# Optimization experiments

Hardware: AMD Instinct MI355X
Metric: run time of the kernel (lower is better)

The kernel has to match this reference:

```python
import jax, jax.numpy as jnp
import numpy as np

NODE_DEG = 9   # SelfAttnAggregation.node_degree: 8 grid neighbors + self loop
PN_EPS = 1e-5  # PyG PairNorm default eps


def _pairnorm(x):
    # PairNorm mode='PN', scale=1: center over nodes, divide by sqrt(mean row sq-norm)
    x = x - x.mean(axis=0, keepdims=True)
    return x / jnp.sqrt(PN_EPS + (x * x).sum(-1).mean())


def _mha(z, qkv_w, qkv_b, out_w, out_b):
    # torch.nn.MultiheadAttention, 1 head, batch_first. z: [N, S, E]
    E = z.shape[-1]
    qkv = jnp.einsum('nse,fe->nsf', z, qkv_w) + qkv_b            # [N, S, 3E]
    q, k, v = jnp.split(qkv, 3, axis=-1)
    scores = jnp.einsum('nse,nte->nst', q, k) / jnp.sqrt(jnp.asarray(E, z.dtype))
    o = jnp.einsum('nst,nte->nse', jax.nn.softmax(scores, axis=-1), v)
    return jnp.einsum('nse,fe->nsf', o, out_w) + out_b


def _gcn_conv(x, W, b, nbr_idx, qkv_w, qkv_b, out_w, out_b):
    # GCNConv(normalize=False, add_self_loops baked into nbr_idx) + SelfAttnAggregation
    h = x @ W                                   # [N, C]
    C = h.shape[-1]
    dense = h[nbr_idx]                          # [N, 9, C]  to_dense_batch gather
    N, S, _ = dense.shape
    pos = jnp.broadcast_to(jnp.eye(S, dtype=h.dtype), (N, S, S))
    z = jnp.concatenate([dense, pos], axis=-1)  # [N, 9, C+9]; pad amount is 0 for deg==9
    z = z + _mha(z, qkv_w[0], qkv_b[0], out_w[0], out_b[0]) \
          + _mha(z, qkv_w[1], qkv_b[1], out_w[1], out_b[1])
    return jnp.max(z[:, :, :C], axis=1) + b     # max-pool over neighbor slots, then bias


def setup_inputs() -> dict:
    key = jax.random.key(0)
    N, HID, W = 32768, 80, 80
    E = W + NODE_DEG  # 89
    ks = jax.random.split(key, 6)
    x = jax.random.normal(ks[0], (N, HID + 2), jnp.float32)
    nbr = jax.random.randint(ks[1], (N, NODE_DEG), 0, N, dtype=jnp.int32)
    nbr = nbr.at[:, -1].set(jnp.arange(N, dtype=jnp.int32))  # add_self_loops=True
    s = 0.05
    return {
        'x': x,
        'W1': jax.random.normal(ks[2], (HID + 2, W), jnp.float32) * s,
        'b1': jnp.zeros((W,), jnp.float32),
        'W2': jax.random.normal(ks[3], (W, W), jnp.float32) * s,
        'b2': jnp.zeros((W,), jnp.float32),
        'attn_qkv_w': jax.random.normal(ks[4], (2, 2, 3 * E, E), jnp.float32) * s,
        'attn_qkv_b': jnp.zeros((2, 2, 3 * E), jnp.float32),
        'attn_out_w': jax.random.normal(ks[5], (2, 2, E, E), jnp.float32) * s,
        'attn_out_b': jnp.zeros((2, 2, E), jnp.float32),
        'nbr_idx': nbr,
    }


def reference(x, W1, b1, W2, b2, attn_qkv_w, attn_qkv_b, attn_out_w, attn_out_b, nbr_idx):
    # UpdateRule.step()
    u = _gcn_conv(x, W1, b1, nbr_idx, attn_qkv_w[0], attn_qkv_b[0], attn_out_w[0], attn_out_b[0])
    u = jax.nn.relu(_pairnorm(u))
    u = _gcn_conv(u, W2, b2, nbr_idx, attn_qkv_w[1], attn_qkv_b[1], attn_out_w[1], attn_out_b[1])
    u = jax.nn.relu(_pairnorm(u))
    out = x[:, :-2] + u                          # residual (drops the 2 flag channels)
    last = out[:, -1]
    last = jnp.where((last > 1.0) | (last < -1.0), 0.0, last)
    out = out.at[:, -1].set(last)
    return out * 0.5
```

## Files before the change

### kernel.cpp

```cpp
#include <hip/hip_runtime.h>

#define NN 32768
#define HWID 448

#define OFF_G     0
#define OFF_M     25600
#define OFF_FF    51200
#define OFF_FG    54080
#define OFF_CC    56960
#define OFF_C2    57284
#define OFF_CW    60164
#define OFF_STATS 133636
#define OFF_MS    133956
#define OFF_H     134148
#define OFF_U     14814212

__global__ __launch_bounds__(256) void k_prep_small(const float* __restrict__ qkvw,
                                                    const float* __restrict__ qkvb,
                                                    const float* __restrict__ outw,
                                                    float* __restrict__ ws) {
    int combo = blockIdx.y;
    int e = blockIdx.x * 256 + threadIdx.x;
    const float* Wq = qkvw + combo * 267 * 89;
    const float* Wk = Wq + 89 * 89;
    const float* Wv = Wq + 178 * 89;
    const float* bq = qkvb + combo * 267;
    const float* bk = bq + 89;
    const float* bv = bq + 178;
    const float* Wo = outw + combo * 89 * 89;
    if (e < 6400) {
        int a = e / 80, b = e % 80;
        float s = 0.f;
        for (int j = 0; j < 89; ++j) s += Wq[j*89+a] * Wk[j*89+b];
        ws[OFF_G + combo*6400 + e] = s;
    } else if (e < 12800) {
        int e2 = e - 6400; int f = e2 / 80, c = e2 % 80;
        float s = 0.f;
        for (int j = 0; j < 89; ++j) s += Wo[f*89+j] * Wv[j*89+c];
        ws[OFF_M + combo*6400 + e2] = s;
    } else if (e < 13520) {
        int e3 = e - 12800; int a = e3 / 9, t = e3 % 9;
        float s = 0.f;
        for (int j = 0; j < 89; ++j) s += Wq[j*89+a] * (Wk[j*89+80+t] + bk[j]);
        ws[OFF_FF + combo*720 + e3] = s;
    } else if (e < 14240) {
        int e4 = e - 13520; int a = e4 / 9, si = e4 % 9;
        float s = 0.f;
        for (int j = 0; j < 89; ++j) s += Wk[j*89+a] * (Wq[j*89+80+si] + bq[j]);
        ws[OFF_FG + combo*720 + e4] = s;
    } else if (e < 14321) {
        int e5 = e - 14240; int si = e5 / 9, t = e5 % 9;
        float s = 0.f;
        for (int j = 0; j < 89; ++j) s += (Wq[j*89+80+si] + bq[j]) * (Wk[j*89+80+t] + bk[j]);
        ws[OFF_CC + combo*81 + e5] = s;
    } else if (e < 15041) {
        int e6 = e - 14321; int t = e6 / 80, f = e6 % 80;
        float s = 0.f;
        for (int j = 0; j < 89; ++j) s += Wo[f*89+j] * (Wv[j*89+80+t] + bv[j]);
        ws[OFF_C2 + combo*720 + e6] = s;
    }
}

__global__ __launch_bounds__(256) void k_prep_cw(const float* __restrict__ W1,
                                                 const float* __restrict__ W2,
                                                 float* __restrict__ ws) {
    int l = blockIdx.y;
    int e = blockIdx.x * 256 + threadIdx.x;
    if (e >= 82 * 448) return;
    int k = e / 448, j = e % 448;
    int K = (l == 0) ? 82 : 80;
    float val = 0.f;
    if (k < K) {
        const float* Wr = ((l == 0) ? W1 : W2) + k * 80;
        if (j < 80) {
            val = Wr[j];
        } else if (j < 240) {
            int m = (j - 80) / 80, col = (j - 80) % 80;
            const float* G = ws + OFF_G + (l*2+m)*6400;
            float s = 0.f;
            for (int c = 0; c < 80; ++c) s += Wr[c] * G[c*80 + col];
            val = s;
        } else if (j < 276) {
            int q = j - 240; int m = q / 18; int qq = q % 18;
            int combo = l*2 + m;
            if (qq < 9) {
                const float* Ff = ws + OFF_FF + combo*720;
                float s = 0.f;
                for (int c = 0; c < 80; ++c) s += Wr[c] * Ff[c*9 + qq];
                val = s;
            } else {
                const float* Fg = ws + OFF_FG + combo*720;
                float s = 0.f;
                for (int c = 0; c < 80; ++c) s += Wr[c] * Fg[c*9 + qq - 9];
                val = s;
            }
        } else if (j >= 280 && j < 440) {
            int m = (j - 280) / 80, f = (j - 280) % 80;
            const float* M = ws + OFF_M + (l*2+m)*6400 + f*80;
            float s = 0.f;
            for (int c = 0; c < 80; ++c) s += Wr[c] * M[c];
            val = s;
        }
    }
    ws[OFF_CW + (size_t)l*82*448 + e] = val;
}

template<int K, bool TRANS>
__global__ __launch_bounds__(256) void k_gemm(const float* __restrict__ A,
                                              const float* __restrict__ CW,
                                              float* __restrict__ H,
                                              const float* __restrict__ ms) {
    __shared__ __align__(16) float AsT[K][72];
    __shared__ __align__(16) float Bs[K][68];
    int tid = threadIdx.x;
    int n0 = blockIdx.x * 64;
    int j0 = blockIdx.y * 64;
    float scale0 = 0.f;
    if constexpr (TRANS) scale0 = ms[80];
    for (int idx = tid; idx < 64 * K; idx += 256) {
        int r = idx / K, k = idx - r * K;
        float v = A[(size_t)(n0 + r) * K + k];
        if constexpr (TRANS) v = fmaxf(0.f, (v - ms[k]) * scale0);
        AsT[k][r] = v;
    }
    for (int idx = tid; idx < K * 16; idx += 256) {
        int k = idx >> 4, c4 = idx & 15;
        *(float4*)(&Bs[k][c4 * 4]) = *(const float4*)(&CW[k * 448 + j0 + c4 * 4]);
    }
    __syncthreads();
    int r0 = (tid >> 4) * 4, c0 = (tid & 15) * 4;
    float acc[4][4] = {};
    #pragma unroll 2
    for (int k = 0; k < K; ++k) {
        float4 a4 = *(const float4*)(&AsT[k][r0]);
        float4 b4 = *(const float4*)(&Bs[k][c0]);
        acc[0][0] += a4.x*b4.x; acc[0][1] += a4.x*b4.y; acc[0][2] += a4.x*b4.z; acc[0][3] += a4.x*b4.w;
        acc[1][0] += a4.y*b4.x; acc[1][1] += a4.y*b4.y; acc[1][2] += a4.y*b4.z; acc[1][3] += a4.y*b4.w;
        acc[2][0] += a4.z*b4.x; acc[2][1] += a4.z*b4.y; acc[2][2] += a4.z*b4.z; acc[2][3] += a4.z*b4.w;
        acc[3][0] += a4.w*b4.x; acc[3][1] += a4.w*b4.y; acc[3][2] += a4.w*b4.z; acc[3][3] += a4.w*b4.w;
    }
    for (int i = 0; i < 4; ++i) {
        float4 v = make_float4(acc[i][0], acc[i][1], acc[i][2], acc[i][3]);
        *(float4*)(&H[(size_t)(n0 + r0 + i) * HWID + j0 + c0]) = v;
    }
}

__global__ __launch_bounds__(128) void k_attn(const float* __restrict__ ws,
                                              const float* __restrict__ Hbuf,
                                              const int* __restrict__ nbr,
                                              const float* __restrict__ outb,
                                              const float* __restrict__ bvec,
                                              float* __restrict__ u,
                                              int l) {
    __shared__ __align__(16) float sS[2][9][242];
    __shared__ float sP[2][2][9][9];
    __shared__ float sCC[2][81];
    int tid = threadIdx.x;
    int wave = tid >> 6, lane = tid & 63;
    int n = blockIdx.x * 2 + wave;
    int nv = nbr[n * 9 + (lane < 9 ? lane : 8)];
    int rr[9];
    #pragma unroll
    for (int s = 0; s < 9; ++s) rr[s] = __shfl(nv, s);

    int s1 = lane / 9, t1 = lane - s1 * 9;
    const float* rowS1 = Hbuf + (size_t)rr[s1] * HWID;
    const float* rowT1 = Hbuf + (size_t)rr[t1] * HWID;
    float f1a = rowS1[240 + t1], g1a = rowT1[249 + s1];
    float f2a = rowS1[258 + t1], g2a = rowT1[267 + s1];
    int pp2 = (lane < 17) ? (lane + 64) : 80;
    int s2 = pp2 / 9, t2 = pp2 - s2 * 9;
    const float* rowS2 = Hbuf + (size_t)rr[s2] * HWID;
    const float* rowT2 = Hbuf + (size_t)rr[t2] * HWID;
    float f1b = rowS2[240 + t2], g1b = rowT2[249 + s2];
    float f2b = rowS2[258 + t2], g2b = rowT2[267 + s2];

    for (int i = tid; i < 162; i += 128) sCC[0][i] = ws[OFF_CC + (l*2)*81 + i];

    float4 st0, st1, st2, st3, st4, st5, st6, st7, st8;
    {
        #define LD_ST(J, DST)                                                   \
        {   int i = lane + 64 * (J);                                            \
            int row = i / 60, c4 = i - row * 60;                                \
            int r = __shfl(nv, row);                                            \
            if (i < 540) DST = *(const float4*)(Hbuf + (size_t)r * HWID + c4 * 4); \
            else DST = make_float4(0.f,0.f,0.f,0.f); }
        LD_ST(0, st0) LD_ST(1, st1) LD_ST(2, st2) LD_ST(3, st3) LD_ST(4, st4)
        LD_ST(5, st5) LD_ST(6, st6) LD_ST(7, st7) LD_ST(8, st8)
        #undef LD_ST
    }
    {
        #define ST_ST(J, SRC)                                                   \
        {   int i = lane + 64 * (J);                                            \
            if (i < 540) {                                                      \
                int row = i / 60, c4 = i - row * 60;                            \
                *(float4*)(&sS[wave][row][c4 * 4]) = SRC; } }
        ST_ST(0, st0) ST_ST(1, st1) ST_ST(2, st2) ST_ST(3, st3) ST_ST(4, st4)
        ST_ST(5, st5) ST_ST(6, st6) ST_ST(7, st7) ST_ST(8, st8)
        #undef ST_ST
    }
    __syncthreads();

    const float rsE = 1.0f / 9.433981132056603f;
    {
        float a0 = 0.f, a1 = 0.f, b0 = 0.f, b1 = 0.f;
        #pragma unroll
        for (int i = 0; i < 20; ++i) {
            float4 hh = *(const float4*)(&sS[wave][t1][4*i]);
            float4 g1 = *(const float4*)(&sS[wave][s1][80 + 4*i]);
            float4 g2 = *(const float4*)(&sS[wave][s1][160 + 4*i]);
            a0 += g1.x*hh.x + g1.y*hh.y; a1 += g1.z*hh.z + g1.w*hh.w;
            b0 += g2.x*hh.x + g2.y*hh.y; b1 += g2.z*hh.z + g2.w*hh.w;
        }
        sP[wave][0][s1][t1] = (a0 + a1 + f1a + g1a + sCC[0][lane]) * rsE;
        sP[wave][1][s1][t1] = (b0 + b1 + f2a + g2a + sCC[1][lane]) * rsE;
    }
    if (lane < 17) {
        float a0 = 0.f, a1 = 0.f, b0 = 0.f, b1 = 0.f;
        #pragma unroll
        for (int i = 0; i < 20; ++i) {
            float4 hh = *(const float4*)(&sS[wave][t2][4*i]);
            float4 g1 = *(const float4*)(&sS[wave][s2][80 + 4*i]);
            float4 g2 = *(const float4*)(&sS[wave][s2][160 + 4*i]);
            a0 += g1.x*hh.x + g1.y*hh.y; a1 += g1.z*hh.z + g1.w*hh.w;
            b0 += g2.x*hh.x + g2.y*hh.y; b1 += g2.z*hh.z + g2.w*hh.w;
        }
        sP[wave][0][s2][t2] = (a0 + a1 + f1b + g1b + sCC[0][pp2]) * rsE;
        sP[wave][1][s2][t2] = (b0 + b1 + f2b + g2b + sCC[1][pp2]) * rsE;
    }
    __syncthreads();
    if (lane < 18) {
        int m = lane / 9, s = lane - m*9;
        float row[9]; float mx = -1e30f;
        #pragma unroll
        for (int t = 0; t < 9; ++t) { row[t] = sP[wave][m][s][t]; mx = fmaxf(mx, row[t]); }
        float sm = 0.f;
        #pragma unroll
        for (int t = 0; t < 9; ++t) { row[t] = __expf(row[t] - mx); sm += row[t]; }
        float inv = 1.f / sm;
        #pragma unroll
        for (int t = 0; t < 9; ++t) sP[wave][m][s][t] = row[t] * inv;
    }
    __syncthreads();
    for (int f = lane; f < 80; f += 64) {
        float acc[9] = {};
        #pragma unroll
        for (int m = 0; m < 2; ++m) {
            const float* c2 = ws + OFF_C2 + (l*2+m)*720;
            #pragma unroll
            for (int t = 0; t < 9; ++t) {
                float vv = Hbuf[(size_t)rr[t]*HWID + 280 + m*80 + f] + c2[t*80 + f];
                #pragma unroll
                for (int s = 0; s < 9; ++s) acc[s] += sP[wave][m][s][t] * vv;
            }
        }
        float mx = -1e30f;
        #pragma unroll
        for (int s = 0; s < 9; ++s) mx = fmaxf(mx, acc[s] + sS[wave][s][f]);
        float bias = outb[(l*2)*89 + f] + outb[(l*2+1)*89 + f] + bvec[f];
        u[(size_t)n*80 + f] = mx + bias;
    }
}

__global__ __launch_bounds__(256) void k_colreduce(const float* __restrict__ u, float* __restrict__ stats) {
    __shared__ float ps[3][80], ps2[3][80];
    int tid = threadIdx.x;
    int c = tid % 80, rg = tid / 80;
    if (rg < 3) {
        float s = 0.f, s2 = 0.f;
        int rbase = blockIdx.x * 48 + rg * 16;
        for (int i = 0; i < 16; ++i) {
            int rw = rbase + i;
            if (rw < NN) {
                float v = u[(size_t)rw*80 + c];
                s += v; s2 += v*v;
            }
        }
        ps[rg][c] = s; ps2[rg][c] = s2;
    }
    __syncthreads();
    if (tid < 80) {
        atomicAdd(&stats[tid],      ps[0][tid] + ps[1][tid] + ps[2][tid]);
        atomicAdd(&stats[80 + tid], ps2[0][tid] + ps2[1][tid] + ps2[2][tid]);
    }
}

__global__ __launch_bounds__(128) void k_normscale(const float* __restrict__ stats, float* __restrict__ ms) {
    __shared__ float red[80];
    int t = threadIdx.x;
    if (t < 80) {
        float mean = stats[t] * (1.0f / (float)NN);
        ms[t] = mean;
        red[t] = stats[80 + t] - (float)NN * mean * mean;
    }
    __syncthreads();
    if (t == 0) {
        float ss = 0.f;
        for (int i = 0; i < 80; ++i) ss += red[i];
        ms[80] = 1.0f / sqrtf(1e-5f + ss * (1.0f / (float)NN));
    }
}

__global__ __launch_bounds__(256) void k_final(const float* __restrict__ x,
                                               const float* __restrict__ u2,
                                               const float* __restrict__ ms,
                                               float* __restrict__ out) {
    int g = blockIdx.x * 256 + threadIdx.x;
    int n = g / 80, f = g % 80;
    float scale0 = ms[80];
    float v = fmaxf(0.f, (u2[g] - ms[f]) * scale0);
    float o = x[(size_t)n*82 + f] + v;
    if (f == 79 && (o > 1.0f || o < -1.0f)) o = 0.f;
    out[g] = o * 0.5f;
}

extern "C" void kernel_launch(void* const* d_in, const int* in_sizes, int n_in,
                              void* d_out, int out_size, void* d_ws, size_t ws_size,
                              hipStream_t stream) {
    const float* x    = (const float*)d_in[0];
    const float* W1   = (const float*)d_in[1];
    const float* b1   = (const float*)d_in[2];
    const float* W2   = (const float*)d_in[3];
    const float* b2   = (const float*)d_in[4];
    const float* qkvw = (const float*)d_in[5];
    const float* qkvb = (const float*)d_in[6];
    const float* outw = (const float*)d_in[7];
    const float* outb = (const float*)d_in[8];
    const int*   nbr  = (const int*)d_in[9];
    float* ws = (float*)d_ws;
    float* out = (float*)d_out;

    float* H = ws + OFF_H;
    float* u = ws + OFF_U;

    hipMemsetAsync(ws + OFF_STATS, 0, 320 * sizeof(float), stream);
    k_prep_small<<<dim3(59, 4), 256, 0, stream>>>(qkvw, qkvb, outw, ws);
    k_prep_cw<<<dim3(144, 2), 256, 0, stream>>>(W1, W2, ws);

    k_gemm<82, false><<<dim3(512, 7), 256, 0, stream>>>(x, ws + OFF_CW, H, nullptr);
    k_attn<<<16384, 128, 0, stream>>>(ws, H, nbr, outb, b1, u, 0);
    k_colreduce<<<683, 256, 0, stream>>>(u, ws + OFF_STATS);
    k_normscale<<<1, 128, 0, stream>>>(ws + OFF_STATS, ws + OFF_MS);

    k_gemm<80, true><<<dim3(512, 7), 256, 0, stream>>>(u, ws + OFF_CW + 82*448, H, ws + OFF_MS);
    k_attn<<<16384, 128, 0, stream>>>(ws, H, nbr, outb, b2, u, 1);
    k_colreduce<<<683, 256, 0, stream>>>(u, ws + OFF_STATS + 160);
    k_normscale<<<1, 128, 0, stream>>>(ws + OFF_STATS + 160, ws + OFF_MS + 96);

    k_final<<<10240, 256, 0, stream>>>(x, u, ws + OFF_MS + 96, out);
}
```

Before: 523.1 us.

## Split attention heads across waves with one node per block in k_attn

The attention kernel now handles one node per 128-thread block instead of two, and each wave computes one of the two attention heads. Gathering the 9 neighbor rows is shared by both waves, each wave computes scores for a single head, and the final stage splits the 80 output features 40 per wave. V-values and bias are loaded into registers before the first barrier so their latency overlaps the shared-memory fill. The launch grid doubles, block-level barriers now couple two waves of the same node, and 24 lanes per wave sit idle in the output stage.

Result: no change. 524.9 us (+0.3%).

```diff
diff --git a/kernel.cpp b/kernel.cpp
--- a/kernel.cpp
+++ b/kernel.cpp
@@ -152,112 +152,113 @@
                                               const float* __restrict__ bvec,
                                               float* __restrict__ u,
                                               int l) {
-    __shared__ __align__(16) float sS[2][9][242];
-    __shared__ float sP[2][2][9][9];
-    __shared__ float sCC[2][81];
+    __shared__ __align__(16) float sS[9][242];
+    __shared__ float sP[2][9][9];
     int tid = threadIdx.x;
-    int wave = tid >> 6, lane = tid & 63;
-    int n = blockIdx.x * 2 + wave;
+    int m = tid >> 6, lane = tid & 63;
+    int n = blockIdx.x;
     int nv = nbr[n * 9 + (lane < 9 ? lane : 8)];
     int rr[9];
     #pragma unroll
     for (int s = 0; s < 9; ++s) rr[s] = __shfl(nv, s);
 
+    int pp2 = (lane < 17) ? (lane + 64) : 80;
     int s1 = lane / 9, t1 = lane - s1 * 9;
+    int s2 = pp2 / 9, t2 = pp2 - s2 * 9;
+
     const float* rowS1 = Hbuf + (size_t)rr[s1] * HWID;
     const float* rowT1 = Hbuf + (size_t)rr[t1] * HWID;
-    float f1a = rowS1[240 + t1], g1a = rowT1[249 + s1];
-    float f2a = rowS1[258 + t1], g2a = rowT1[267 + s1];
-    int pp2 = (lane < 17) ? (lane + 64) : 80;
-    int s2 = pp2 / 9, t2 = pp2 - s2 * 9;
+    float fa = rowS1[240 + 18*m + t1], ga = rowT1[249 + 18*m + s1];
     const float* rowS2 = Hbuf + (size_t)rr[s2] * HWID;
     const float* rowT2 = Hbuf + (size_t)rr[t2] * HWID;
-    float f1b = rowS2[240 + t2], g1b = rowT2[249 + s2];
-    float f2b = rowS2[258 + t2], g2b = rowT2[267 + s2];
-
-    for (int i = tid; i < 162; i += 128) sCC[0][i] = ws[OFF_CC + (l*2)*81 + i];
-
-    float4 st0, st1, st2, st3, st4, st5, st6, st7, st8;
+    float fb = rowS2[240 + 18*m + t2], gb = rowT2[249 + 18*m + s2];
+
+    float cca = ws[OFF_CC + (l*2 + m)*81 + lane];
+    float ccb = ws[OFF_CC + (l*2 + m)*81 + pp2];
+
+    float4 st0, st1, st2, st3, st4;
     {
         #define LD_ST(J, DST)                                                   \
-        {   int i = lane + 64 * (J);                                            \
+        {   int i = tid + 128 * (J);                                            \
             int row = i / 60, c4 = i - row * 60;                                \
-            int r = __shfl(nv, row);                                            \
-            if (i < 540) DST = *(const float4*)(Hbuf + (size_t)r * HWID + c4 * 4); \
-            else DST = make_float4(0.f,0.f,0.f,0.f); }
+            if (i < 540) {                                                      \
+                int r = __shfl(nv, row);                                        \
+                DST = *(const float4*)(Hbuf + (size_t)r * HWID + c4 * 4);       \
+            } else DST = make_float4(0.f,0.f,0.f,0.f); }
         LD_ST(0, st0) LD_ST(1, st1) LD_ST(2, st2) LD_ST(3, st3) LD_ST(4, st4)
-        LD_ST(5, st5) LD_ST(6, st6) LD_ST(7, st7) LD_ST(8, st8)
         #undef LD_ST
     }
     {
         #define ST_ST(J, SRC)                                                   \
-        {   int i = lane + 64 * (J);                                            \
+        {   int i = tid + 128 * (J);                                            \
             if (i < 540) {                                                      \
                 int row = i / 60, c4 = i - row * 60;                            \
-                *(float4*)(&sS[wave][row][c4 * 4]) = SRC; } }
+                *(float4*)(&sS[row][c4 * 4]) = SRC; } }
         ST_ST(0, st0) ST_ST(1, st1) ST_ST(2, st2) ST_ST(3, st3) ST_ST(4, st4)
-        ST_ST(5, st5) ST_ST(6, st6) ST_ST(7, st7) ST_ST(8, st8)
         #undef ST_ST
     }
+
+    int f = 40*m + ((lane < 40) ? lane : 39);
+    const float* c20 = ws + OFF_C2 + (l*2)*720;
+    const float* c21 = c20 + 720;
+    float v0[9], v1[9];
+    #pragma unroll
+    for (int t = 0; t < 9; ++t) {
+        const float* rowp = Hbuf + (size_t)rr[t] * HWID + 280;
+        v0[t] = rowp[f]      + c20[t*80 + f];
+        v1[t] = rowp[80 + f] + c21[t*80 + f];
+    }
+    float bias = outb[(l*2)*89 + f] + outb[(l*2+1)*89 + f] + bvec[f];
+
     __syncthreads();
 
     const float rsE = 1.0f / 9.433981132056603f;
+    int goff = 80 + 80*m;
     {
-        float a0 = 0.f, a1 = 0.f, b0 = 0.f, b1 = 0.f;
+        float a0 = 0.f, a1 = 0.f;
         #pragma unroll
         for (int i = 0; i < 20; ++i) {
-            float4 hh = *(const float4*)(&sS[wave][t1][4*i]);
-            float4 g1 = *(const float4*)(&sS[wave][s1][80 + 4*i]);
-            float4 g2 = *(const float4*)(&sS[wave][s1][160 + 4*i]);
-            a0 += g1.x*hh.x + g1.y*hh.y; a1 += g1.z*hh.z + g1.w*hh.w;
-            b0 += g2.x*hh.x + g2.y*hh.y; b1 += g2.z*hh.z + g2.w*hh.w;
-        }
-        sP[wave][0][s1][t1] = (a0 + a1 + f1a + g1a + sCC[0][lane]) * rsE;
-        sP[wave][1][s1][t1] = (b0 + b1 + f2a + g2a + sCC[1][lane]) * rsE;
+            float4 hh = *(const float4*)(&sS[t1][4*i]);
+            float4 gg = *(const float4*)(&sS[s1][goff + 4*i]);
+            a0 += gg.x*hh.x + gg.y*hh.y; a1 += gg.z*hh.z + gg.w*hh.w;
+        }
+        sP[m][s1][t1] = (a0 + a1 + fa + ga + cca) * rsE;
     }
     if (lane < 17) {
-        float a0 = 0.f, a1 = 0.f, b0 = 0.f, b1 = 0.f;
+        float a0 = 0.f, a1 = 0.f;
         #pragma unroll
         for (int i = 0; i < 20; ++i) {
-            float4 hh = *(const float4*)(&sS[wave][t2][4*i]);
-            float4 g1 = *(const float4*)(&sS[wave][s2][80 + 4*i]);
-            float4 g2 = *(const float4*)(&sS[wave][s2][160 + 4*i]);
-            a0 += g1.x*hh.x + g1.y*hh.y; a1 += g1.z*hh.z + g1.w*hh.w;
-            b0 += g2.x*hh.x + g2.y*hh.y; b1 += g2.z*hh.z + g2.w*hh.w;
-        }
-        sP[wave][0][s2][t2] = (a0 + a1 + f1b + g1b + sCC[0][pp2]) * rsE;
-        sP[wave][1][s2][t2] = (b0 + b1 + f2b + g2b + sCC[1][pp2]) * rsE;
-    }
-    __syncthreads();
-    if (lane < 18) {
-        int m = lane / 9, s = lane - m*9;
+            float4 hh = *(const float4*)(&sS[t2][4*i]);
+            float4 gg = *(const float4*)(&sS[s2][goff + 4*i]);
+            a0 += gg.x*hh.x + gg.y*hh.y; a1 += gg.z*hh.z + gg.w*hh.w;
+        }
+        sP[m][s2][t2] = (a0 + a1 + fb + gb + ccb) * rsE;
+    }
+    __syncthreads();
+    if (lane < 9) {
+        int s = lane;
         float row[9]; float mx = -1e30f;
         #pragma unroll
-        for (int t = 0; t < 9; ++t) { row[t] = sP[wave][m][s][t]; mx = fmaxf(mx, row[t]); }
+        for (int t = 0; t < 9; ++t) { row[t] = sP[m][s][t]; mx = fmaxf(mx, row[t]); }
         float sm = 0.f;
         #pragma unroll
         for (int t = 0; t < 9; ++t) { row[t] = __expf(row[t] - mx); sm += row[t]; }
         float inv = 1.f / sm;
         #pragma unroll
-        for (int t = 0; t < 9; ++t) sP[wave][m][s][t] = row[t] * inv;
-    }
-    __syncthreads();
-    for (int f = lane; f < 80; f += 64) {
+        for (int t = 0; t < 9; ++t) sP[m][s][t] = row[t] * inv;
+    }
+    __syncthreads();
+    if (lane < 40) {
         float acc[9] = {};
         #pragma unroll
-        for (int m = 0; m < 2; ++m) {
-            const float* c2 = ws + OFF_C2 + (l*2+m)*720;
+        for (int t = 0; t < 9; ++t) {
+            float a = v0[t], b = v1[t];
             #pragma unroll
-            for (int t = 0; t < 9; ++t) {
-                float vv = Hbuf[(size_t)rr[t]*HWID + 280 + m*80 + f] + c2[t*80 + f];
-                #pragma unroll
-                for (int s = 0; s < 9; ++s) acc[s] += sP[wave][m][s][t] * vv;
-            }
+            for (int s = 0; s < 9; ++s) acc[s] += sP[0][s][t] * a + sP[1][s][t] * b;
         }
         float mx = -1e30f;
         #pragma unroll
-        for (int s = 0; s < 9; ++s) mx = fmaxf(mx, acc[s] + sS[wave][s][f]);
-        float bias = outb[(l*2)*89 + f] + outb[(l*2+1)*89 + f] + bvec[f];
+        for (int s = 0; s < 9; ++s) mx = fmaxf(mx, acc[s] + sS[s][f]);
         u[(size_t)n*80 + f] = mx + bias;
     }
 }
@@ -338,12 +339,12 @@
     k_prep_cw<<<dim3(144, 2), 256, 0, stream>>>(W1, W2, ws);
 
     k_gemm<82, false><<<dim3(512, 7), 256, 0, stream>>>(x, ws + OFF_CW, H, nullptr);
-    k_attn<<<16384, 128, 0, stream>>>(ws, H, nbr, outb, b1, u, 0);
+    k_attn<<<32768, 128, 0, stream>>>(ws, H, nbr, outb, b1, u, 0);
     k_colreduce<<<683, 256, 0, stream>>>(u, ws + OFF_STATS);
     k_normscale<<<1, 128, 0, stream>>>(ws + OFF_STATS, ws + OFF_MS);
 
     k_gemm<80, true><<<dim3(512, 7), 256, 0, stream>>>(u, ws + OFF_CW + 82*448, H, ws + OFF_MS);
-    k_attn<<<16384, 128, 0, stream>>>(ws, H, nbr, outb, b2, u, 1);
+    k_attn<<<32768, 128, 0, stream>>>(ws, H, nbr, outb, b2, u, 1);
     k_colreduce<<<683, 256, 0, stream>>>(u, ws + OFF_STATS + 160);
     k_normscale<<<1, 128, 0, stream>>>(ws + OFF_STATS + 160, ws + OFF_MS + 96);
 
```
